# Performance work log

Measured on AMD Instinct MI355X. Metric: run time of the kernel, lower is better.

The kernel has to match this reference:

```python
import jax, jax.numpy as jnp
import numpy as np

# Faithful emulation of SQBnBLinear: SmoothQuant rescale fused with
# bnb Linear8bitLt (threshold=0.0 => no fp16 outlier path):
#   w_sq = weight / scales ; x_sq = x * scales
#   row-wise absmax int8 quantization of both x (per token) and w (per out row)
#   int8 GEMM, then dequant with (ax * aw / 127^2), plus bias / scales.

B, S, D = 4, 2048, 4096

def setup_inputs() -> dict:
    key = jax.random.key(0)
    k1, k2, k3, k4 = jax.random.split(key, 4)
    x = jax.random.normal(k1, (B, S, D), dtype=jnp.float32)
    weight = jax.random.normal(k2, (D, D), dtype=jnp.float32) * 0.02
    bias = jax.random.normal(k3, (D,), dtype=jnp.float32) * 0.02
    # SmoothQuant scales are positive per-input-channel factors
    scales = jax.random.uniform(k4, (D,), dtype=jnp.float32, minval=0.5, maxval=2.0)
    return {"x": x, "weight": weight, "bias": bias, "scales": scales}

def _quantize_rowwise(t):
    # symmetric per-row (last-dim) absmax int8 quantization
    absmax = jnp.max(jnp.abs(t), axis=-1, keepdims=True)
    absmax = jnp.maximum(absmax, 1e-8)
    q = jnp.clip(jnp.round(t * (127.0 / absmax)), -127.0, 127.0)
    return q, absmax

def reference(x, weight, bias, scales):
    # __init__: fold SmoothQuant scales into weight and bias
    w_sq = weight / scales            # [out, in] / [in]
    b_sq = bias / scales              # valid because in_features == out_features
    # forward: rescale input (mul_ by scales)
    x_sq = x * scales                 # [B, S, in]
    # LLM.int8() with threshold=0.0: pure int8 path
    qx, ax = _quantize_rowwise(x_sq)  # qx [B,S,in], ax [B,S,1]
    qw, aw = _quantize_rowwise(w_sq)  # qw [out,in], aw [out,1]
    acc = jnp.einsum('bsi,oi->bso', qx, qw)  # int accumulate (emulated in fp32)
    out = acc * (ax / 127.0) * (aw[:, 0] / 127.0) + b_sq
    return out
```

## Files before the change

kernel.cpp:

```cpp
#include <hip/hip_runtime.h>
#include <stdint.h>

#define DDIM 4096
#define MTOK 8192

typedef __attribute__((ext_vector_type(4))) int i32x4;

__device__ __forceinline__ void async16(const void* g, void* l) {
    __builtin_amdgcn_global_load_lds(
        (const __attribute__((address_space(1))) unsigned int*)g,
        (__attribute__((address_space(3))) unsigned int*)l,
        16, 0, 0);
}

__global__ __launch_bounds__(256) void quant_all(
    const float* __restrict__ x, const float* __restrict__ weight,
    const float* __restrict__ scales,
    signed char* __restrict__ qx, float* __restrict__ sx,
    signed char* __restrict__ qw, float* __restrict__ sw,
    const float* __restrict__ bias, float* __restrict__ bq)
{
    __shared__ float red[4];
    const int tid = threadIdx.x;
    const bool is_x = blockIdx.x < MTOK;
    const int row = is_x ? blockIdx.x : (blockIdx.x - MTOK);
    const float* src = is_x ? (x + (size_t)row * DDIM) : (weight + (size_t)row * DDIM);
    signed char* q = is_x ? qx : qw;
    float* srow = is_x ? sx : sw;

    const float4* s4 = (const float4*)scales;
    const float4* x4 = (const float4*)src;

    float4 v[4];
    float am = 0.0f;
#pragma unroll
    for (int j = 0; j < 4; ++j) {
        float4 a = x4[tid + j * 256];
        float4 s = s4[tid + j * 256];
        float4 r;
        if (is_x) { r.x = a.x * s.x; r.y = a.y * s.y; r.z = a.z * s.z; r.w = a.w * s.w; }
        else      { r.x = a.x / s.x; r.y = a.y / s.y; r.z = a.z / s.z; r.w = a.w / s.w; }
        v[j] = r;
        am = fmaxf(am, fmaxf(fmaxf(fabsf(r.x), fabsf(r.y)),
                             fmaxf(fabsf(r.z), fabsf(r.w))));
    }
#pragma unroll
    for (int off = 32; off > 0; off >>= 1)
        am = fmaxf(am, __shfl_xor(am, off, 64));
    if ((tid & 63) == 0) red[tid >> 6] = am;
    __syncthreads();
    am = fmaxf(fmaxf(red[0], red[1]), fmaxf(red[2], red[3]));
    am = fmaxf(am, 1e-8f);

    const float sc = 127.0f / am;
    uint32_t* qrow = (uint32_t*)(q + (size_t)row * DDIM);
#pragma unroll
    for (int j = 0; j < 4; ++j) {
        int q0 = (int)fminf(127.0f, fmaxf(-127.0f, rintf(v[j].x * sc)));
        int q1 = (int)fminf(127.0f, fmaxf(-127.0f, rintf(v[j].y * sc)));
        int q2 = (int)fminf(127.0f, fmaxf(-127.0f, rintf(v[j].z * sc)));
        int q3 = (int)fminf(127.0f, fmaxf(-127.0f, rintf(v[j].w * sc)));
        qrow[tid + j * 256] = (uint32_t)(q0 & 0xff) | ((uint32_t)(q1 & 0xff) << 8) |
                              ((uint32_t)(q2 & 0xff) << 16) | ((uint32_t)(q3 & 0xff) << 24);
    }
    if (tid == 0) {
        srow[row] = am * (1.0f / 127.0f);
        if (!is_x) bq[row] = bias[row] / scales[row];
    }
}

__global__ __launch_bounds__(256) void gemm_i8(
    const signed char* __restrict__ qx, const signed char* __restrict__ qw,
    const float* __restrict__ sx, const float* __restrict__ sw,
    const float* __restrict__ bq, float* __restrict__ out)
{
    __shared__ __align__(16) signed char sA[128 * 64];
    __shared__ __align__(16) signed char sB[128 * 64];

    const int K = DDIM, N = DDIM;
    const int tid  = threadIdx.x;
    const int bm   = blockIdx.y;
    const int bn   = blockIdx.x;
    const int wave = tid >> 6;
    const int lane = tid & 63;
    const int wm   = (wave & 1) << 6;
    const int wn   = (wave >> 1) << 6;
    const int l16  = lane & 15;
    const int quad = lane >> 4;

    const signed char* Ab = qx + (size_t)bm * 128 * K;
    const signed char* Bb = qw + (size_t)bn * 128 * K;

    const int l0 = tid * 16;
    const int r0 = l0 >> 6;
    const int g0 = ((((l0 >> 4) & 3) ^ ((r0 >> 1) & 3)) << 4);
    const int l1 = l0 + 4096;
    const int r1 = l1 >> 6;
    const int g1 = ((((l1 >> 4) & 3) ^ ((r1 >> 1) & 3)) << 4);

    const int rchunk = ((quad ^ ((l16 >> 1) & 3)) << 4);

    i32x4 acc[4][4] = {};

    for (int k0 = 0; k0 < K; k0 += 64) {
        async16(Ab + (size_t)r0 * K + k0 + g0, &sA[l0]);
        async16(Ab + (size_t)r1 * K + k0 + g1, &sA[l1]);
        async16(Bb + (size_t)r0 * K + k0 + g0, &sB[l0]);
        async16(Bb + (size_t)r1 * K + k0 + g1, &sB[l1]);
        __syncthreads();

        i32x4 a[4], b[4];
#pragma unroll
        for (int i = 0; i < 4; ++i)
            a[i] = *(const i32x4*)&sA[(wm + i * 16 + l16) * 64 + rchunk];
#pragma unroll
        for (int j = 0; j < 4; ++j)
            b[j] = *(const i32x4*)&sB[(wn + j * 16 + l16) * 64 + rchunk];

#pragma unroll
        for (int i = 0; i < 4; ++i)
#pragma unroll
            for (int j = 0; j < 4; ++j)
                acc[i][j] = __builtin_amdgcn_mfma_i32_16x16x64_i8(a[i], b[j], acc[i][j], 0, 0, 0);

        __syncthreads();
    }

#pragma unroll
    for (int i = 0; i < 4; ++i) {
#pragma unroll
        for (int j = 0; j < 4; ++j) {
            const int n = bn * 128 + wn + j * 16 + l16;
            const float swn = sw[n];
            const float bqn = bq[n];
#pragma unroll
            for (int r = 0; r < 4; ++r) {
                const int m = bm * 128 + wm + i * 16 + quad * 4 + r;
                out[(size_t)m * N + n] = (float)acc[i][j][r] * sx[m] * swn + bqn;
            }
        }
    }
}

extern "C" void kernel_launch(void* const* d_in, const int* in_sizes, int n_in,
                              void* d_out, int out_size, void* d_ws, size_t ws_size,
                              hipStream_t stream) {
    const float* x      = (const float*)d_in[0];
    const float* weight = (const float*)d_in[1];
    const float* bias   = (const float*)d_in[2];
    const float* scales = (const float*)d_in[3];
    float* out = (float*)d_out;

    char* ws = (char*)d_ws;
    signed char* qx = (signed char*)ws;
    signed char* qw = (signed char*)(ws + 33554432);
    float* sx = (float*)(ws + 50331648);
    float* sw = (float*)(ws + 50364416);
    float* bq = (float*)(ws + 50380800);

    quant_all<<<MTOK + DDIM, 256, 0, stream>>>(x, weight, scales, qx, sx, qw, sw, bias, bq);

    dim3 grid(DDIM / 128, MTOK / 128);
    gemm_i8<<<grid, 256, 0, stream>>>(qx, qw, sx, sw, bq, out);
}
```

Measured before the change: 431.6 us.

## Switch int8 GEMM to 32x32x32 MFMA with 128-wide K tiles

```diff
diff --git a/kernel.cpp b/kernel.cpp
--- a/kernel.cpp
+++ b/kernel.cpp
@@ -5,6 +5,7 @@
 #define MTOK 8192
 
 typedef __attribute__((ext_vector_type(4))) int i32x4;
+typedef __attribute__((ext_vector_type(16))) int i32x16;
 
 __device__ __forceinline__ void async16(const void* g, void* l) {
     __builtin_amdgcn_global_load_lds(
@@ -74,8 +75,8 @@
     const float* __restrict__ sx, const float* __restrict__ sw,
     const float* __restrict__ bq, float* __restrict__ out)
 {
-    __shared__ __align__(16) signed char sA[128 * 64];
-    __shared__ __align__(16) signed char sB[128 * 64];
+    __shared__ __align__(16) signed char sA[128 * 128];
+    __shared__ __align__(16) signed char sB[128 * 128];
 
     const int K = DDIM, N = DDIM;
     const int tid  = threadIdx.x;
@@ -85,58 +86,60 @@
     const int lane = tid & 63;
     const int wm   = (wave & 1) << 6;
     const int wn   = (wave >> 1) << 6;
-    const int l16  = lane & 15;
-    const int quad = lane >> 4;
+    const int r5   = lane & 31;
+    const int hi   = lane >> 5;
 
     const signed char* Ab = qx + (size_t)bm * 128 * K;
     const signed char* Bb = qw + (size_t)bn * 128 * K;
 
-    const int l0 = tid * 16;
-    const int r0 = l0 >> 6;
-    const int g0 = ((((l0 >> 4) & 3) ^ ((r0 >> 1) & 3)) << 4);
-    const int l1 = l0 + 4096;
-    const int r1 = l1 >> 6;
-    const int g1 = ((((l1 >> 4) & 3) ^ ((r1 >> 1) & 3)) << 4);
+    const int srow0 = tid >> 3;
+    const int cir   = tid & 7;
 
-    const int rchunk = ((quad ^ ((l16 >> 1) & 3)) << 4);
+    int roff[4];
+#pragma unroll
+    for (int kq = 0; kq < 4; ++kq)
+        roff[kq] = (((kq * 2 + hi) ^ (r5 & 7)) << 4);
 
-    i32x4 acc[4][4] = {};
+    i32x16 acc[2][2] = {};
 
-    for (int k0 = 0; k0 < K; k0 += 64) {
-        async16(Ab + (size_t)r0 * K + k0 + g0, &sA[l0]);
-        async16(Ab + (size_t)r1 * K + k0 + g1, &sA[l1]);
-        async16(Bb + (size_t)r0 * K + k0 + g0, &sB[l0]);
-        async16(Bb + (size_t)r1 * K + k0 + g1, &sB[l1]);
+    for (int k0 = 0; k0 < K; k0 += 128) {
+#pragma unroll
+        for (int c = 0; c < 4; ++c) {
+            const int row = srow0 + 32 * c;
+            const int kc  = cir ^ (row & 7);
+            const int p   = tid * 16 + c * 4096;
+            async16(Ab + (size_t)row * K + k0 + kc * 16, &sA[p]);
+            async16(Bb + (size_t)row * K + k0 + kc * 16, &sB[p]);
+        }
         __syncthreads();
 
-        i32x4 a[4], b[4];
 #pragma unroll
-        for (int i = 0; i < 4; ++i)
-            a[i] = *(const i32x4*)&sA[(wm + i * 16 + l16) * 64 + rchunk];
-#pragma unroll
-        for (int j = 0; j < 4; ++j)
-            b[j] = *(const i32x4*)&sB[(wn + j * 16 + l16) * 64 + rchunk];
-
-#pragma unroll
-        for (int i = 0; i < 4; ++i)
-#pragma unroll
-            for (int j = 0; j < 4; ++j)
-                acc[i][j] = __builtin_amdgcn_mfma_i32_16x16x64_i8(a[i], b[j], acc[i][j], 0, 0, 0);
+        for (int kq = 0; kq < 4; ++kq) {
+            i32x4 a0 = *(const i32x4*)&sA[(wm +      r5) * 128 + roff[kq]];
+            i32x4 a1 = *(const i32x4*)&sA[(wm + 32 + r5) * 128 + roff[kq]];
+            i32x4 b0 = *(const i32x4*)&sB[(wn +      r5) * 128 + roff[kq]];
+            i32x4 b1 = *(const i32x4*)&sB[(wn + 32 + r5) * 128 + roff[kq]];
+            acc[0][0] = __builtin_amdgcn_mfma_i32_32x32x32_i8(a0, b0, acc[0][0], 0, 0, 0);
+            acc[0][1] = __builtin_amdgcn_mfma_i32_32x32x32_i8(a0, b1, acc[0][1], 0, 0, 0);
+            acc[1][0] = __builtin_amdgcn_mfma_i32_32x32x32_i8(a1, b0, acc[1][0], 0, 0, 0);
+            acc[1][1] = __builtin_amdgcn_mfma_i32_32x32x32_i8(a1, b1, acc[1][1], 0, 0, 0);
+        }
 
         __syncthreads();
     }
 
 #pragma unroll
-    for (int i = 0; i < 4; ++i) {
+    for (int mi = 0; mi < 2; ++mi) {
 #pragma unroll
-        for (int j = 0; j < 4; ++j) {
-            const int n = bn * 128 + wn + j * 16 + l16;
+        for (int nj = 0; nj < 2; ++nj) {
+            const int n = bn * 128 + wn + nj * 32 + r5;
             const float swn = sw[n];
             const float bqn = bq[n];
+            const int mbase = bm * 128 + wm + mi * 32 + 4 * hi;
 #pragma unroll
-            for (int r = 0; r < 4; ++r) {
-                const int m = bm * 128 + wm + i * 16 + quad * 4 + r;
-                out[(size_t)m * N + n] = (float)acc[i][j][r] * sx[m] * swn + bqn;
+            for (int r = 0; r < 16; ++r) {
+                const int m = mbase + (r & 3) + 8 * (r >> 2);
+                out[(size_t)m * N + n] = (float)acc[mi][nj][r] * sx[m] * swn + bqn;
             }
         }
     }
```

Measured after the change: 417.4 us. -3.3%, faster.
